# Kernel tuning notes

Measured on AMD Instinct MI355X. Metric: run time of the kernel, lower is better.

Reference implementation:

```python
import jax, jax.numpy as jnp
import numpy as np

INPUT_DIM = 1024; HID = 512; DSTATE = 64; EXPAND = 2; HDIM = 32; NHEAD = 8; DFF = 1024
DIN = EXPAND * HID          # 1024 inner dim
NH = DIN // HDIM            # 32 heads
G = 1; DCONV = 4            # ngroups, depthwise conv kernel
CONV_DIM = DIN + 2 * G * DSTATE          # 1152 (x, B, C go through conv)
DPROJ = 2 * DIN + 2 * G * DSTATE + NH    # 2208 (z, xBC, dt)
B = 2; L = 4096


def rmsnorm(x, w, eps=1e-5):
    return x * jax.lax.rsqrt(jnp.mean(x * x, axis=-1, keepdims=True) + eps) * w


def layernorm(x, w, b, eps=1e-5):
    m = jnp.mean(x, axis=-1, keepdims=True)
    v = jnp.mean((x - m) ** 2, axis=-1, keepdims=True)
    return (x - m) * jax.lax.rsqrt(v + eps) * w + b


def mamba_block(x, Wi, cw, cb, dtb, Alog, Dp, nw, Wo):
    # Mamba-2 style selective scan block (SISO, ngroups=1)
    Bb, Ln, _ = x.shape
    zxbcdt = x @ Wi                                   # [B,L,DPROJ]
    z = zxbcdt[..., :DIN]
    xBC = zxbcdt[..., DIN:DIN + CONV_DIM]
    dt = zxbcdt[..., DIN + CONV_DIM:]                 # [B,L,NH]
    # causal depthwise conv1d + silu
    xBC = jnp.transpose(xBC, (0, 2, 1))               # [B,C,L]
    xBC = jax.lax.conv_general_dilated(xBC, cw, (1,), [(DCONV - 1, 0)],
                                       feature_group_count=CONV_DIM) + cb[None, :, None]
    xBC = jax.nn.silu(jnp.transpose(xBC, (0, 2, 1)))
    xs = xBC[..., :DIN].reshape(Bb, Ln, NH, HDIM)     # [B,L,H,P]
    Bm = xBC[..., DIN:DIN + DSTATE]                   # [B,L,N]
    Cm = xBC[..., DIN + DSTATE:]                      # [B,L,N]
    dt = jax.nn.softplus(dt + dtb)                    # [B,L,H]
    decay = jnp.exp(dt * (-jnp.exp(Alog)))            # [B,L,H]
    dtx = dt[..., None] * xs                          # [B,L,H,P]

    def step(h, inp):
        dec, dx, Bt, Ct = inp                         # [B,H],[B,H,P],[B,N],[B,N]
        h = h * dec[:, :, None, None] + dx[..., None] * Bt[:, None, None, :]
        return h, jnp.einsum('bhpn,bn->bhp', h, Ct)

    h0 = jnp.zeros((Bb, NH, HDIM, DSTATE), x.dtype)
    _, ys = jax.lax.scan(step, h0, (jnp.moveaxis(decay, 1, 0), jnp.moveaxis(dtx, 1, 0),
                                    jnp.moveaxis(Bm, 1, 0), jnp.moveaxis(Cm, 1, 0)))
    y = jnp.moveaxis(ys, 0, 1) + Dp[None, None, :, None] * xs
    y = y.reshape(Bb, Ln, DIN)
    return rmsnorm(y * jax.nn.silu(z), nw) @ Wo       # gated RMSNorm + out proj


def transformer_layer(x, Wqkv, bqkv, Wo, bo, W1, b1, W2, b2, ln1w, ln1b, ln2w, ln2b):
    Bb, Ln, Dm = x.shape
    hd = Dm // NHEAD
    qkv = x @ Wqkv + bqkv
    q, k, v = jnp.split(qkv, 3, axis=-1)
    sp = lambda t: t.reshape(Bb, Ln, NHEAD, hd).transpose(0, 2, 1, 3)
    q, k, v = sp(q), sp(k), sp(v)
    att = jax.nn.softmax(jnp.einsum('bhqd,bhkd->bhqk', q, k) / np.float32(np.sqrt(hd)), axis=-1)
    o = jnp.einsum('bhqk,bhkd->bhqd', att, v).transpose(0, 2, 1, 3).reshape(Bb, Ln, Dm)
    x = layernorm(x + o @ Wo + bo, ln1w, ln1b)
    ff = jax.nn.gelu(x @ W1 + b1, approximate=False) @ W2 + b2
    return layernorm(x + ff, ln2w, ln2b)


def setup_inputs() -> dict:
    key = jax.random.key(0)
    ks = iter(jax.random.split(key, 64))
    w = lambda shape, s=0.02: jax.random.normal(next(ks), shape, jnp.float32) * s
    d = {}
    d['x'] = jax.random.normal(next(ks), (B, L, INPUT_DIM), jnp.float32)
    d['Wp'] = w((INPUT_DIM, HID)); d['bp'] = jnp.zeros((HID,), jnp.float32)
    for p in ('m1', 'm2'):
        d[p + '_Wi'] = w((HID, DPROJ))
        d[p + '_cw'] = w((CONV_DIM, 1, DCONV), 0.2)
        d[p + '_cb'] = jnp.zeros((CONV_DIM,), jnp.float32)
        d[p + '_dtb'] = jnp.log(jnp.expm1(jax.random.uniform(next(ks), (NH,), jnp.float32, 0.001, 0.1)))
        d[p + '_Alog'] = jnp.log(jax.random.uniform(next(ks), (NH,), jnp.float32, 1.0, 16.0))
        d[p + '_D'] = jnp.ones((NH,), jnp.float32)
        d[p + '_nw'] = jnp.ones((DIN,), jnp.float32)
        d[p + '_Wo'] = w((DIN, HID))
    d['n1_w'] = jnp.ones((HID,), jnp.float32); d['n2_w'] = jnp.ones((HID,), jnp.float32)
    d['ds_w'] = w((HID, HID, 3)); d['ds_b'] = jnp.zeros((HID,), jnp.float32)
    d['t_Wqkv'] = w((HID, 3 * HID)); d['t_bqkv'] = jnp.zeros((3 * HID,), jnp.float32)
    d['t_Wo'] = w((HID, HID)); d['t_bo'] = jnp.zeros((HID,), jnp.float32)
    d['t_W1'] = w((HID, DFF)); d['t_b1'] = jnp.zeros((DFF,), jnp.float32)
    d['t_W2'] = w((DFF, HID)); d['t_b2'] = jnp.zeros((HID,), jnp.float32)
    d['t_ln1w'] = jnp.ones((HID,), jnp.float32); d['t_ln1b'] = jnp.zeros((HID,), jnp.float32)
    d['t_ln2w'] = jnp.ones((HID,), jnp.float32); d['t_ln2b'] = jnp.zeros((HID,), jnp.float32)
    d['on_w'] = jnp.ones((HID,), jnp.float32); d['on_b'] = jnp.zeros((HID,), jnp.float32)
    return d


def reference(x, Wp, bp,
              m1_Wi, m1_cw, m1_cb, m1_dtb, m1_Alog, m1_D, m1_nw, m1_Wo,
              m2_Wi, m2_cw, m2_cb, m2_dtb, m2_Alog, m2_D, m2_nw, m2_Wo,
              n1_w, n2_w, ds_w, ds_b,
              t_Wqkv, t_bqkv, t_Wo, t_bo, t_W1, t_b1, t_W2, t_b2,
              t_ln1w, t_ln1b, t_ln2w, t_ln2b, on_w, on_b):
    x = x @ Wp + bp
    x = rmsnorm(mamba_block(x, m1_Wi, m1_cw, m1_cb, m1_dtb, m1_Alog, m1_D, m1_nw, m1_Wo) + x, n1_w)
    x = rmsnorm(mamba_block(x, m2_Wi, m2_cw, m2_cb, m2_dtb, m2_Alog, m2_D, m2_nw, m2_Wo) + x, n2_w)
    xt = jnp.transpose(x, (0, 2, 1))                  # [B,HID,L]
    xt = jax.lax.conv_general_dilated(xt, ds_w, (2,), [(1, 1)]) + ds_b[None, :, None]
    x = jnp.transpose(xt, (0, 2, 1))                  # [B,L/2,HID]
    x = transformer_layer(x, t_Wqkv, t_bqkv, t_Wo, t_bo, t_W1, t_b1, t_W2, t_b2,
                          t_ln1w, t_ln1b, t_ln2w, t_ln2b)
    return layernorm(x, on_w, on_b)
```

## Files before the change

### kernel.cpp

```cpp
#include <hip/hip_runtime.h>
#include <math.h>

#define DIN_   1024
#define DSTATE_ 64
#define NH_    32
#define HDIM_  32
#define CONVD_ 1152
#define DPROJ_ 2208
#define HID_   512
#define LSEQ_  4096
#define BB_    2
#define LT_    2048
#define NHEAD_ 8
#define HD_    64
#define DFF_   1024
#define LC_    256
#define NC_    16
#define NS_    2
#define KTS_   (LT_ / 64 / NS_)

typedef __attribute__((ext_vector_type(8))) short bf16x8;
typedef __attribute__((ext_vector_type(4))) short s16x4;
typedef __attribute__((ext_vector_type(4))) float f32x4;

__device__ __forceinline__ float siluf(float x) { return x / (1.f + __expf(-x)); }

__device__ __forceinline__ short f2b(float f) {
  union { float f; unsigned u; } v; v.f = f;
  unsigned r = (v.u + 0x7fffu + ((v.u >> 16) & 1u)) >> 16;
  return (short)r;
}

__device__ __forceinline__ short f2bt(float f) {
  union { float f; unsigned u; } v; v.f = f;
  return (short)(v.u >> 16);
}

__device__ __forceinline__ float b2f(short s) {
  union { unsigned u; float f; } v; v.u = ((unsigned)(unsigned short)s) << 16;
  return v.f;
}

__device__ __forceinline__ void gload16(const short* g, short* lds_base) {
#if __has_builtin(__builtin_amdgcn_global_load_lds)
  __builtin_amdgcn_global_load_lds((const __attribute__((address_space(1))) void*)g,
                                   (__attribute__((address_space(3))) void*)lds_base, 16, 0, 0);
#else
  int l = threadIdx.x & 63;
  ((bf16x8*)lds_base)[l] = *(const bf16x8*)g;
#endif
}

__device__ __forceinline__ void xcd_swz(int& bx, int& by, int& bz) {
  int nbx = gridDim.x, nby = gridDim.y;
  int nwg = nbx * nby * gridDim.z;
  int orig = (blockIdx.z * nby + blockIdx.y) * nbx + blockIdx.x;
  int q = nwg >> 3, r = nwg & 7;
  int xcd = orig & 7, lin = orig >> 3;
  int wg = (xcd < r ? xcd * (q + 1) : r * (q + 1) + (xcd - r) * q) + lin;
  bx = wg % nbx; wg /= nbx;
  by = wg % nby;
  bz = wg / nby;
}

__global__ void ec_f2b(const float* __restrict__ in, short* __restrict__ out, int n8)
{
  int i = blockIdx.x * 256 + threadIdx.x;
  if (i >= n8) return;
  const float4* p = (const float4*)(in + (size_t)i * 8);
  float4 a = p[0], b = p[1];
  bf16x8 o;
  o[0] = f2b(a.x); o[1] = f2b(a.y); o[2] = f2b(a.z); o[3] = f2b(a.w);
  o[4] = f2b(b.x); o[5] = f2b(b.y); o[6] = f2b(b.z); o[7] = f2b(b.w);
  *(bf16x8*)(out + (size_t)i * 8) = o;
}

__global__ __launch_bounds__(256) void ec_w2bt(const float* __restrict__ W,
                                               short* __restrict__ Wt, int K, int N)
{
  __shared__ float t[32][33];
  int k0 = blockIdx.x * 32, n0 = blockIdx.y * 32;
  int tx = threadIdx.x & 31, ty = threadIdx.x >> 5;
#pragma unroll
  for (int i = 0; i < 32; i += 8) t[ty + i][tx] = W[(size_t)(k0 + ty + i) * N + n0 + tx];
  __syncthreads();
#pragma unroll
  for (int i = 0; i < 32; i += 8) Wt[(size_t)(n0 + ty + i) * K + k0 + tx] = f2b(t[tx][ty + i]);
}

__global__ void ec_dswt(const float* __restrict__ w, short* __restrict__ wt)
{
  int idx = blockIdx.x * 256 + threadIdx.x;
  if (idx >= HID_ * 1536) return;
  int o = idx / 1536, r = idx % 1536;
  int k = r >> 9, i = r & 511;
  wt[idx] = f2b(w[((size_t)o * HID_ + i) * 3 + k]);
}

__global__ void ec_cwt(const float* __restrict__ cw, float* __restrict__ cwt)
{
  int idx = blockIdx.x * 256 + threadIdx.x;
  if (idx >= CONVD_ * 4) return;
  int j = idx / CONVD_, c = idx % CONVD_;
  cwt[idx] = cw[c * 4 + j];
}

__global__ __launch_bounds__(256) void ec_gemm16b(
    const short* __restrict__ A, const short* __restrict__ Wt,
    const float* __restrict__ bias, const float* __restrict__ res,
    float* __restrict__ Cf, short* __restrict__ Ch,
    int M, int N, int K, int act, int lda, long Az, int Mz)
{
  __shared__ short As_[2][2048];
  __shared__ short Bs_[2][2048];
  int bxi, byi, bzi;
  xcd_swz(bxi, byi, bzi);
  A += (size_t)bzi * Az;
  const int mz = bzi * Mz;
  const int tid = threadIdx.x;
  const int l = tid & 63, w = tid >> 6;
  const int m0 = byi * 64, n0 = bxi * 64;
  const int wm = (w >> 1) * 32, wn = (w & 1) * 32;
  const int lr = l & 15, lk = l >> 4;
  const int arow = l >> 2, acol = (l & 3) * 8;

  f32x4 acc[2][2];
#pragma unroll
  for (int i = 0; i < 2; ++i)
#pragma unroll
    for (int j = 0; j < 2; ++j) acc[i][j] = f32x4{0.f, 0.f, 0.f, 0.f};

  {
    const short* ga = A + (size_t)(m0 + w * 16 + arow) * lda + acol;
    int rb = n0 + w * 16 + arow; if (rb > N - 1) rb = N - 1;
    const short* gb = Wt + (size_t)rb * K + acol;
    gload16(ga, &As_[0][w * 512]);
    gload16(gb, &Bs_[0][w * 512]);
  }

  const int KT = K >> 5;
  for (int kt = 0; kt < KT; ++kt) {
    __syncthreads();
    if (kt + 1 < KT) {
      int k0 = (kt + 1) << 5;
      int nb = (kt + 1) & 1;
      const short* ga = A + (size_t)(m0 + w * 16 + arow) * lda + k0 + acol;
      int rb = n0 + w * 16 + arow; if (rb > N - 1) rb = N - 1;
      const short* gb = Wt + (size_t)rb * K + k0 + acol;
      gload16(ga, &As_[nb][w * 512]);
      gload16(gb, &Bs_[nb][w * 512]);
    }
    int cb = kt & 1;
    bf16x8 af[2], bfv[2];
#pragma unroll
    for (int mf = 0; mf < 2; ++mf)
      af[mf] = *(const bf16x8*)&As_[cb][(wm + mf * 16 + lr) * 32 + lk * 8];
#pragma unroll
    for (int nf = 0; nf < 2; ++nf)
      bfv[nf] = *(const bf16x8*)&Bs_[cb][(wn + nf * 16 + lr) * 32 + lk * 8];
#pragma unroll
    for (int mf = 0; mf < 2; ++mf)
#pragma unroll
      for (int nf = 0; nf < 2; ++nf)
        acc[mf][nf] = __builtin_amdgcn_mfma_f32_16x16x32_bf16(af[mf], bfv[nf], acc[mf][nf], 0, 0, 0);
  }

#pragma unroll
  for (int mf = 0; mf < 2; ++mf)
#pragma unroll
    for (int nf = 0; nf < 2; ++nf)
#pragma unroll
      for (int r = 0; r < 4; ++r) {
        int m = mz + m0 + wm + mf * 16 + lk * 4 + r;
        int n = n0 + wn + nf * 16 + lr;
        if (n < N) {
          float v = acc[mf][nf][r];
          if (bias) v += bias[n];
          if (act == 1) v = 0.5f * v * (1.f + erff(v * 0.70710678118f));
          if (res) v += res[(size_t)m * N + n];
          if (Cf) Cf[(size_t)m * N + n] = v;
          if (Ch) Ch[(size_t)m * N + n] = f2b(v);
        }
      }
}

static inline void gemm16b(hipStream_t s, const short* A, const short* Wt, const float* bias,
                           const float* res, float* Cf, short* Ch, int M, int N, int K, int act) {
  dim3 g((N + 63) / 64, M / 64), b(256);
  ec_gemm16b<<<g, b, 0, s>>>(A, Wt, bias, res, Cf, Ch, M, N, K, act, K, 0, 0);
}

__global__ __launch_bounds__(512) void ec_dsfix(
    const short* __restrict__ x16, const short* __restrict__ wt,
    const float* __restrict__ bias, float* __restrict__ dsf, short* __restrict__ ds16)
{
  const int b = blockIdx.x, o = threadIdx.x;
  float v = bias[o];
#pragma unroll
  for (int k = 1; k < 3; ++k) {
    const short* xr = x16 + ((size_t)b * LSEQ_ + (k - 1)) * HID_;
    const short* wr = wt + (size_t)o * 1536 + k * 512;
    for (int i = 0; i < 512; ++i) v += b2f(xr[i]) * b2f(wr[i]);
  }
  dsf[(size_t)b * LT_ * HID_ + o] = v;
  ds16[(size_t)b * LT_ * HID_ + o] = f2b(v);
}

__global__ __launch_bounds__(256) void ec_conv1d_silu(
    const short* __restrict__ zx16, const float* __restrict__ cwt,
    const float* __restrict__ cb, short* __restrict__ xbc16,
    short* __restrict__ B16, short* __restrict__ C16)
{
  int idx = blockIdx.x * 256 + threadIdx.x;
  const int NG = CONVD_ / 4;
  if (idx >= BB_ * LSEQ_ * NG) return;
  int cg = idx % NG;
  int row = idx / NG;
  int l = row & (LSEQ_ - 1);
  int c0 = cg * 4;
  float4 cbv = *(const float4*)(cb + c0);
  float a0 = cbv.x, a1 = cbv.y, a2 = cbv.z, a3 = cbv.w;
#pragma unroll
  for (int j = 0; j < 4; ++j) {
    int ll = l - 3 + j;
    if (ll >= 0) {
      s16x4 xv = *(const s16x4*)(zx16 + (size_t)(row + ll - l) * DPROJ_ + DIN_ + c0);
      float4 wv = *(const float4*)(cwt + j * CONVD_ + c0);
      a0 += b2f(xv[0]) * wv.x;
      a1 += b2f(xv[1]) * wv.y;
      a2 += b2f(xv[2]) * wv.z;
      a3 += b2f(xv[3]) * wv.w;
    }
  }
  a0 = siluf(a0); a1 = siluf(a1); a2 = siluf(a2); a3 = siluf(a3);
  s16x4 pk; pk[0] = f2b(a0); pk[1] = f2b(a1); pk[2] = f2b(a2); pk[3] = f2b(a3);
  *(s16x4*)(xbc16 + (size_t)row * CONVD_ + c0) = pk;
  if (c0 >= DIN_) {
    int col = c0 - DIN_;
    if (col < 64) *(s16x4*)(B16 + (size_t)row * 64 + col) = pk;
    else          *(s16x4*)(C16 + (size_t)row * 64 + col - 64) = pk;
  }
}

__global__ __launch_bounds__(256) void ec_ssd_cumsum(
    const short* __restrict__ zx16, const float* __restrict__ dtb,
    const float* __restrict__ Alog, float* __restrict__ dts,
    float* __restrict__ lp, float* __restrict__ Pc)
{
  const int c = blockIdx.x, b = blockIdx.y, hg = blockIdx.z;
  const int t = threadIdx.x;
  const int lane = t & 63, wv = t >> 6;
  const size_t row = (size_t)b * LSEQ_ + (size_t)c * LC_ + t;
  const int h0 = hg * 8;
  __shared__ float wsum[4][8];

  bf16x8 dv = *(const bf16x8*)(zx16 + row * DPROJ_ + (DIN_ + CONVD_) + h0);
  float dt[8], cs[8];
#pragma unroll
  for (int j = 0; j < 8; ++j) {
    float x = b2f(dv[j]) + dtb[h0 + j];
    float sp = (x > 20.f) ? x : log1pf(__expf(x));
    dt[j] = sp;
    cs[j] = sp;
  }
#pragma unroll
  for (int d = 1; d < 64; d <<= 1) {
#pragma unroll
    for (int j = 0; j < 8; ++j) {
      float o = __shfl_up(cs[j], d, 64);
      if (lane >= d) cs[j] += o;
    }
  }
  if (lane == 63)
#pragma unroll
    for (int j = 0; j < 8; ++j) wsum[wv][j] = cs[j];
  __syncthreads();
#pragma unroll
  for (int j = 0; j < 8; ++j) {
    float base = 0.f;
#pragma unroll
    for (int k = 0; k < 3; ++k) if (k < wv) base += wsum[k][j];
    cs[j] += base;
  }
#pragma unroll
  for (int j = 0; j < 8; ++j) {
    int h = h0 + j;
    float lpv = -expf(Alog[h]) * cs[j];
    dts[row * NH_ + h] = dt[j];
    lp[row * NH_ + h] = lpv;
    if (t == LC_ - 1) Pc[(b * NC_ + c) * NH_ + h] = expf(lpv);
  }
}

__global__ __launch_bounds__(64) void ec_vt(
    const short* __restrict__ xbc16, const float* __restrict__ dts, short* __restrict__ VT)
{
  const int h = blockIdx.x, c = blockIdx.y, b = blockIdx.z;
  const int l = threadIdx.x;
  const size_t rowB = (size_t)b * LSEQ_ + (size_t)c * LC_;
  const size_t vtbase = (size_t)((b * NC_ + c) * NH_ + h) * 32;
  __shared__ float tile[32][33];
  for (int tt = 0; tt < 8; ++tt) {
#pragma unroll
    for (int i = 0; i < 16; ++i) {
      int r = i * 2 + (l >> 5);
      size_t row = rowB + tt * 32 + r;
      tile[r][l & 31] = b2f(xbc16[row * CONVD_ + h * 32 + (l & 31)]) * dts[row * NH_ + h];
    }
    __syncthreads();
#pragma unroll
    for (int j = 0; j < 16; ++j) {
      int p = j * 2 + (l >> 5);
      VT[(vtbase + p) * 256 + tt * 32 + (l & 31)] = f2b(tile[l & 31][p]);
    }
    __syncthreads();
  }
}

__device__ __forceinline__ float* state_ptr(float* stbuf, int b, int c, int h, int e)
{
  return stbuf + ((size_t)((b * NC_ + c) * NH_ + h)) * 2048 + e;
}

__global__ __launch_bounds__(64) void ec_ssd_p1(
    const short* __restrict__ B16, const short* __restrict__ VT,
    const float* __restrict__ lp, float* __restrict__ stbuf)
{
  const int h = blockIdx.x, c = blockIdx.y, b = blockIdx.z;
  const int l = threadIdx.x, lr = l & 15, lk = l >> 4;
  const size_t rowB = (size_t)b * LSEQ_ + (size_t)c * LC_;
  const size_t vtbase = (size_t)((b * NC_ + c) * NH_ + h) * 32;
  __shared__ short BT[64][264];
  for (int i = 0; i < 4; ++i) {
    int t = i * 64 + l;
#pragma unroll
    for (int g = 0; g < 8; ++g) {
      bf16x8 v = *(const bf16x8*)&B16[(rowB + t) * 64 + g * 8];
#pragma unroll
      for (int j = 0; j < 8; ++j) BT[g * 8 + j][t] = v[j];
    }
  }
  __syncthreads();
  const float lpE = lp[(rowB + LC_ - 1) * NH_ + h];
  f32x4 acc[2][4];
#pragma unroll
  for (int i = 0; i < 2; ++i)
#pragma unroll
    for (int j = 0; j < 4; ++j) acc[i][j] = f32x4{0.f, 0.f, 0.f, 0.f};

  for (int ks = 0; ks < 8; ++ks) {
    float wv[8];
#pragma unroll
    for (int j = 0; j < 8; ++j) {
      int t = ks * 32 + lk * 8 + j;
      wv[j] = __expf(lpE - lp[(rowB + t) * NH_ + h]);
    }
    bf16x8 af[2];
#pragma unroll
    for (int mf = 0; mf < 2; ++mf) {
      bf16x8 v = *(const bf16x8*)&VT[(vtbase + mf * 16 + lr) * 256 + ks * 32 + lk * 8];
#pragma unroll
      for (int j = 0; j < 8; ++j) af[mf][j] = f2b(b2f(v[j]) * wv[j]);
    }
#pragma unroll
    for (int nf = 0; nf < 4; ++nf) {
      bf16x8 bf = *(const bf16x8*)&BT[nf * 16 + lr][ks * 32 + lk * 8];
#pragma unroll
      for (int mf = 0; mf < 2; ++mf)
        acc[mf][nf] = __builtin_amdgcn_mfma_f32_16x16x32_bf16(af[mf], bf, acc[mf][nf], 0, 0, 0);
    }
  }
#pragma unroll
  for (int mf = 0; mf < 2; ++mf)
#pragma unroll
    for (int nf = 0; nf < 4; ++nf)
#pragma unroll
      for (int r = 0; r < 4; ++r) {
        int p = mf * 16 + lk * 4 + r, n = nf * 16 + lr;
        *state_ptr(stbuf, b, c, h, p * 64 + n) = acc[mf][nf][r];
      }
}

__global__ __launch_bounds__(512) void ec_scan_p2(
    float* __restrict__ stbuf, const float* __restrict__ Pc)
{
  const int h = blockIdx.x, b = blockIdx.y;
  const int tid = threadIdx.x;
  const int e = (tid >> 4) * 64 + (tid & 15) * 4;
  float h0 = 0.f, h1 = 0.f, h2 = 0.f, h3 = 0.f;
  for (int c = 0; c < NC_; ++c) {
    float* ptr = state_ptr(stbuf, b, c, h, e);
    float4 S = *(float4*)ptr;
    *(float4*)ptr = make_float4(h0, h1, h2, h3);
    float P = Pc[(b * NC_ + c) * NH_ + h];
    h0 = h0 * P + S.x;
    h1 = h1 * P + S.y;
    h2 = h2 * P + S.z;
    h3 = h3 * P + S.w;
  }
}

__global__ __launch_bounds__(256) void ec_ssd_p3(
    const short* __restrict__ B16, const short* __restrict__ C16,
    const short* __restrict__ VT, const float* __restrict__ lp,
    const short* __restrict__ xbc16, const float* __restrict__ Dp,
    float* __restrict__ stbuf, short* __restrict__ y16)
{
  const int h = blockIdx.x, c = blockIdx.y, b = blockIdx.z;
  const int tid = threadIdx.x;
  const int w = tid >> 6, l = tid & 63, lr = l & 15, lk = l >> 4;
  const size_t rowB = (size_t)b * LSEQ_ + (size_t)c * LC_;
  const size_t vtbase = (size_t)((b * NC_ + c) * NH_ + h) * 32;
  __shared__ short hI[32][72];
  __shared__ short Pl[4][64][72];

  for (int i = tid; i < 2048; i += 256)
    hI[i >> 6][i & 63] = f2b(*state_ptr(stbuf, b, c, h, i));
  __syncthreads();

  const int t0 = w * 64;
  bf16x8 cf[4][2];
#pragma unroll
  for (int tf = 0; tf < 4; ++tf)
#pragma unroll
    for (int ks = 0; ks < 2; ++ks)
      cf[tf][ks] = *(const bf16x8*)&C16[(rowB + t0 + tf * 16 + lr) * 64 + ks * 32 + lk * 8];

  f32x4 Y[4][2];
#pragma unroll
  for (int i = 0; i < 4; ++i)
#pragma unroll
    for (int j = 0; j < 2; ++j) Y[i][j] = f32x4{0.f, 0.f, 0.f, 0.f};
#pragma unroll
  for (int nf = 0; nf < 2; ++nf)
#pragma unroll
    for (int ks = 0; ks < 2; ++ks) {
      bf16x8 hf = *(const bf16x8*)&hI[nf * 16 + lr][ks * 32 + lk * 8];
#pragma unroll
      for (int mf = 0; mf < 4; ++mf)
        Y[mf][nf] = __builtin_amdgcn_mfma_f32_16x16x32_bf16(cf[mf][ks], hf, Y[mf][nf], 0, 0, 0);
    }
#pragma unroll
  for (int mf = 0; mf < 4; ++mf)
#pragma unroll
    for (int r = 0; r < 4; ++r) {
      float e = __expf(lp[(rowB + t0 + mf * 16 + lk * 4 + r) * NH_ + h]);
      Y[mf][0][r] *= e;
      Y[mf][1][r] *= e;
    }
  float tlp[4];
#pragma unroll
  for (int tf = 0; tf < 4; ++tf)
    tlp[tf] = lp[(rowB + t0 + tf * 16 + lr) * NH_ + h];

  for (int st = 0; st <= w; ++st) {
    const int s0 = st * 64;
#pragma unroll
    for (int half = 0; half < 2; ++half) {
      f32x4 ST[2][4];
#pragma unroll
      for (int i = 0; i < 2; ++i)
#pragma unroll
        for (int j = 0; j < 4; ++j) ST[i][j] = f32x4{0.f, 0.f, 0.f, 0.f};
#pragma unroll
      for (int sf2 = 0; sf2 < 2; ++sf2) {
        int sf = half * 2 + sf2;
#pragma unroll
        for (int ks = 0; ks < 2; ++ks) {
          bf16x8 bfr = *(const bf16x8*)&B16[(rowB + s0 + sf * 16 + lr) * 64 + ks * 32 + lk * 8];
#pragma unroll
          for (int tf = 0; tf < 4; ++tf)
            ST[sf2][tf] = __builtin_amdgcn_mfma_f32_16x16x32_bf16(bfr, cf[tf][ks], ST[sf2][tf], 0, 0, 0);
        }
      }
#pragma unroll
      for (int sf2 = 0; sf2 < 2; ++sf2) {
        int sf = half * 2 + sf2;
        float slp[4];
#pragma unroll
        for (int r = 0; r < 4; ++r)
          slp[r] = lp[(rowB + s0 + sf * 16 + lk * 4 + r) * NH_ + h];
#pragma unroll
        for (int tf = 0; tf < 4; ++tf) {
          float pv[4];
#pragma unroll
          for (int r = 0; r < 4; ++r) {
            pv[r] = ST[sf2][tf][r] * __expf(tlp[tf] - slp[r]);
            if (st == w && (sf * 16 + lk * 4 + r) > (tf * 16 + lr)) pv[r] = 0.f;
          }
          union { float f; unsigned u; } q0, q1, q2, q3;
          q0.f = pv[0]; q1.f = pv[1]; q2.f = pv[2]; q3.f = pv[3];
          uint2 pk;
          pk.x = (q0.u >> 16) | (q1.u & 0xffff0000u);
          pk.y = (q2.u >> 16) | (q3.u & 0xffff0000u);
          *(uint2*)&Pl[w][tf * 16 + lr][sf * 16 + lk * 4] = pk;
        }
      }
    }
    __builtin_amdgcn_sched_barrier(0);
    asm volatile("s_waitcnt lgkmcnt(0)" ::: "memory");
    __builtin_amdgcn_sched_barrier(0);
#pragma unroll
    for (int ks = 0; ks < 2; ++ks) {
      bf16x8 vf[2];
#pragma unroll
      for (int nf = 0; nf < 2; ++nf)
        vf[nf] = *(const bf16x8*)&VT[(vtbase + nf * 16 + lr) * 256 + s0 + ks * 32 + lk * 8];
#pragma unroll
      for (int mf = 0; mf < 4; ++mf) {
        bf16x8 pf = *(const bf16x8*)&Pl[w][mf * 16 + lr][ks * 32 + lk * 8];
#pragma unroll
        for (int nf = 0; nf < 2; ++nf)
          Y[mf][nf] = __builtin_amdgcn_mfma_f32_16x16x32_bf16(pf, vf[nf], Y[mf][nf], 0, 0, 0);
      }
    }
  }
  const float Dh = Dp[h];
#pragma unroll
  for (int mf = 0; mf < 4; ++mf)
#pragma unroll
    for (int r = 0; r < 4; ++r) {
      size_t yrow = rowB + t0 + mf * 16 + lk * 4 + r;
#pragma unroll
      for (int nf = 0; nf < 2; ++nf) {
        float xv = b2f(xbc16[yrow * CONVD_ + h * 32 + nf * 16 + lr]);
        y16[yrow * DIN_ + h * 32 + nf * 16 + lr] = f2b(Y[mf][nf][r] + Dh * xv);
      }
    }
}

__global__ __launch_bounds__(256) void ec_gate_rms16(
    const short* __restrict__ y16, const short* __restrict__ zx16,
    const float* __restrict__ nw, short* __restrict__ out)
{
  const int row = blockIdx.x;
  const int c0 = threadIdx.x * 4;
  s16x4 yv = *(const s16x4*)(y16 + (size_t)row * DIN_ + c0);
  s16x4 zv = *(const s16x4*)(zx16 + (size_t)row * DPROJ_ + c0);
  float v[4]; float ss = 0.f;
#pragma unroll
  for (int j = 0; j < 4; ++j) {
    float t = b2f(yv[j]) * siluf(b2f(zv[j]));
    v[j] = t; ss += t * t;
  }
#pragma unroll
  for (int m = 32; m >= 1; m >>= 1) ss += __shfl_xor(ss, m, 64);
  __shared__ float buf[4];
  if ((threadIdx.x & 63) == 0) buf[threadIdx.x >> 6] = ss;
  __syncthreads();
  ss = buf[0] + buf[1] + buf[2] + buf[3];
  float scale = rsqrtf(ss / (float)DIN_ + 1e-5f);
  float4 wv = *(const float4*)(nw + c0);
  s16x4 ov;
  ov[0] = f2b(v[0] * scale * wv.x);
  ov[1] = f2b(v[1] * scale * wv.y);
  ov[2] = f2b(v[2] * scale * wv.z);
  ov[3] = f2b(v[3] * scale * wv.w);
  *(s16x4*)(out + (size_t)row * DIN_ + c0) = ov;
}

__global__ __launch_bounds__(128) void ec_rmsadd16(
    const float* __restrict__ a, const float* __restrict__ bres,
    const float* __restrict__ w, float* __restrict__ out, short* __restrict__ out16)
{
  const int row = blockIdx.x;
  const float* ar = a + (size_t)row * HID_;
  const float* br = bres + (size_t)row * HID_;
  float v[4]; float ss = 0.f;
#pragma unroll
  for (int j = 0; j < 4; ++j) {
    int c = j * 128 + threadIdx.x;
    float t = ar[c] + br[c];
    v[j] = t; ss += t * t;
  }
#pragma unroll
  for (int m = 32; m >= 1; m >>= 1) ss += __shfl_xor(ss, m, 64);
  __shared__ float buf[2];
  if ((threadIdx.x & 63) == 0) buf[threadIdx.x >> 6] = ss;
  __syncthreads();
  ss = buf[0] + buf[1];
  float scale = rsqrtf(ss / (float)HID_ + 1e-5f);
#pragma unroll
  for (int j = 0; j < 4; ++j) {
    int c = j * 128 + threadIdx.x;
    float o = v[j] * scale * w[c];
    out[(size_t)row * HID_ + c] = o;
    out16[(size_t)row * HID_ + c] = f2b(o);
  }
}

__global__ __launch_bounds__(128) void ec_ln16(
    const float* __restrict__ in, const float* __restrict__ w,
    const float* __restrict__ bb, float* __restrict__ out, short* __restrict__ out16)
{
  const int row = blockIdx.x;
  const float* ir = in + (size_t)row * HID_;
  float v[4]; float s = 0.f, s2 = 0.f;
#pragma unroll
  for (int j = 0; j < 4; ++j) {
    int c = j * 128 + threadIdx.x;
    float t = ir[c];
    v[j] = t; s += t; s2 += t * t;
  }
#pragma unroll
  for (int m = 32; m >= 1; m >>= 1) { s += __shfl_xor(s, m, 64); s2 += __shfl_xor(s2, m, 64); }
  __shared__ float buf[4];
  if ((threadIdx.x & 63) == 0) { int wi = threadIdx.x >> 6; buf[wi * 2] = s; buf[wi * 2 + 1] = s2; }
  __syncthreads();
  s = buf[0] + buf[2]; s2 = buf[1] + buf[3];
  float mean = s / (float)HID_;
  float var = s2 / (float)HID_ - mean * mean;
  float inv = rsqrtf(var + 1e-5f);
#pragma unroll
  for (int j = 0; j < 4; ++j) {
    int c = j * 128 + threadIdx.x;
    float o = (v[j] - mean) * inv * w[c] + bb[c];
    out[(size_t)row * HID_ + c] = o;
    if (out16) out16[(size_t)row * HID_ + c] = f2b(o);
  }
}

__global__ __launch_bounds__(256) void ec_attn16(
    const short* __restrict__ qkv, float* __restrict__ Op, float2* __restrict__ ml)
{
  const int b = blockIdx.z & 1, split = blockIdx.z >> 1;
  const int h = blockIdx.y, qt = blockIdx.x;
  __shared__ short Kl[64 * 68];
  __shared__ short Vl[64 * 68];
  __shared__ short Pl[64 * 68];
  const int tid = threadIdx.x;
  const int l = tid & 63, w = tid >> 6;
  const int lr = l & 15, lk = l >> 4;

  const size_t qrow = (size_t)b * LT_ + qt * 64 + w * 16 + lr;
  bf16x8 qf[2];
  qf[0] = *(const bf16x8*)&qkv[qrow * 1536 + h * HD_ + lk * 8];
  qf[1] = *(const bf16x8*)&qkv[qrow * 1536 + h * HD_ + lk * 8 + 32];

  float mrun[4] = {-INFINITY, -INFINITY, -INFINITY, -INFINITY};
  float lsum[4] = {0.f, 0.f, 0.f, 0.f};
  f32x4 O[4];
#pragma unroll
  for (int df = 0; df < 4; ++df) O[df] = f32x4{0.f, 0.f, 0.f, 0.f};

  const int krow = tid >> 2, kcg = (tid & 3) * 16;
  const int vd = tid & 63, vw = tid >> 6;

  for (int kt = split * KTS_; kt < (split + 1) * KTS_; ++kt) {
    const size_t krbase = (size_t)b * LT_ + kt * 64;
    {
      const short* kp = &qkv[(krbase + krow) * 1536 + HID_ + h * HD_ + kcg];
      *(bf16x8*)&Kl[krow * 68 + kcg] = *(const bf16x8*)kp;
      *(bf16x8*)&Kl[krow * 68 + kcg + 8] = *(const bf16x8*)(kp + 8);
    }
#pragma unroll
    for (int kk = 0; kk < 4; ++kk) {
      int key0 = vw * 16 + kk * 4;
      s16x4 pk;
#pragma unroll
      for (int j = 0; j < 4; ++j)
        pk[j] = qkv[(krbase + key0 + j) * 1536 + 2 * HID_ + h * HD_ + vd];
      *(s16x4*)&Vl[vd * 68 + key0] = pk;
    }
    __syncthreads();

    f32x4 S[4];
#pragma unroll
    for (int nf = 0; nf < 4; ++nf) S[nf] = f32x4{0.f, 0.f, 0.f, 0.f};
#pragma unroll
    for (int ks = 0; ks < 2; ++ks)
#pragma unroll
      for (int nf = 0; nf < 4; ++nf) {
        bf16x8 kb = *(const bf16x8*)&Kl[(nf * 16 + lr) * 68 + ks * 32 + lk * 8];
        S[nf] = __builtin_amdgcn_mfma_f32_16x16x32_bf16(qf[ks], kb, S[nf], 0, 0, 0);
      }

    float fr[4];
#pragma unroll
    for (int r = 0; r < 4; ++r) {
      float mt = fmaxf(fmaxf(S[0][r], S[1][r]), fmaxf(S[2][r], S[3][r])) * 0.125f;
      mt = fmaxf(mt, __shfl_xor(mt, 1));
      mt = fmaxf(mt, __shfl_xor(mt, 2));
      mt = fmaxf(mt, __shfl_xor(mt, 4));
      mt = fmaxf(mt, __shfl_xor(mt, 8));
      float mn = fmaxf(mrun[r], mt);
      fr[r] = __expf(mrun[r] - mn);
      mrun[r] = mn;
      lsum[r] *= fr[r];
    }
#pragma unroll
    for (int nf = 0; nf < 4; ++nf)
#pragma unroll
      for (int r = 0; r < 4; ++r) {
        float p = __expf(S[nf][r] * 0.125f - mrun[r]);
        lsum[r] += p;
        Pl[(w * 16 + lk * 4 + r) * 68 + nf * 16 + lr] = f2bt(p);
      }
#pragma unroll
    for (int df = 0; df < 4; ++df) {
      O[df][0] *= fr[0]; O[df][1] *= fr[1]; O[df][2] *= fr[2]; O[df][3] *= fr[3];
    }

#pragma unroll
    for (int ks = 0; ks < 2; ++ks) {
      bf16x8 pa = *(const bf16x8*)&Pl[(w * 16 + lr) * 68 + ks * 32 + lk * 8];
#pragma unroll
      for (int df = 0; df < 4; ++df) {
        bf16x8 vb = *(const bf16x8*)&Vl[(df * 16 + lr) * 68 + ks * 32 + lk * 8];
        O[df] = __builtin_amdgcn_mfma_f32_16x16x32_bf16(pa, vb, O[df], 0, 0, 0);
      }
    }
    __syncthreads();
  }

#pragma unroll
  for (int r = 0; r < 4; ++r) {
    lsum[r] += __shfl_xor(lsum[r], 1);
    lsum[r] += __shfl_xor(lsum[r], 2);
    lsum[r] += __shfl_xor(lsum[r], 4);
    lsum[r] += __shfl_xor(lsum[r], 8);
  }
  const size_t sstride = (size_t)BB_ * NHEAD_ * LT_;
  const size_t obase = (size_t)split * sstride + ((size_t)b * NHEAD_ + h) * LT_ + qt * 64 + w * 16;
#pragma unroll
  for (int df = 0; df < 4; ++df)
#pragma unroll
    for (int r = 0; r < 4; ++r)
      Op[(obase + lk * 4 + r) * 64 + df * 16 + lr] = O[df][r];
  if (lr == 0)
#pragma unroll
    for (int r = 0; r < 4; ++r)
      ml[obase + lk * 4 + r] = make_float2(mrun[r], lsum[r]);
}

__global__ __launch_bounds__(256) void ec_attn_comb(
    const float* __restrict__ Op, const float2* __restrict__ ml, short* __restrict__ out)
{
  const int qt = blockIdx.x, h = blockIdx.y, b = blockIdx.z;
  const int r = threadIdx.x >> 2, c0 = (threadIdx.x & 3) * 16;
  const int qrow = qt * 64 + r;
  const size_t sstride = (size_t)BB_ * NHEAD_ * LT_;
  const size_t rb = ((size_t)b * NHEAD_ + h) * LT_ + qrow;
  float m[NS_], lv[NS_];
  float mmax = -INFINITY;
#pragma unroll
  for (int s = 0; s < NS_; ++s) {
    float2 v = ml[rb + s * sstride];
    m[s] = v.x; lv[s] = v.y;
    mmax = fmaxf(mmax, m[s]);
  }
  float den = 0.f, wsc[NS_];
#pragma unroll
  for (int s = 0; s < NS_; ++s) { wsc[s] = __expf(m[s] - mmax); den += lv[s] * wsc[s]; }
  float inv = 1.f / den;
  float o[16];
#pragma unroll
  for (int i = 0; i < 16; ++i) o[i] = 0.f;
#pragma unroll
  for (int s = 0; s < NS_; ++s) {
    const float* p = Op + (rb + s * sstride) * 64 + c0;
    float wq = wsc[s];
#pragma unroll
    for (int i = 0; i < 4; ++i) {
      float4 v = *(const float4*)(p + i * 4);
      o[i * 4 + 0] += v.x * wq; o[i * 4 + 1] += v.y * wq;
      o[i * 4 + 2] += v.z * wq; o[i * 4 + 3] += v.w * wq;
    }
  }
  short* op = out + ((size_t)b * LT_ + qrow) * HID_ + h * HD_ + c0;
#pragma unroll
  for (int i = 0; i < 16; ++i) op[i] = f2b(o[i] * inv);
}

extern "C" void kernel_launch(void* const* d_in, const int* in_sizes, int n_in,
                              void* d_out, int out_size, void* d_ws, size_t ws_size,
                              hipStream_t stream)
{
  const float* x_in   = (const float*)d_in[0];
  const float* Wp     = (const float*)d_in[1];
  const float* bp     = (const float*)d_in[2];
  const float* m_Wi[2]   = {(const float*)d_in[3],  (const float*)d_in[11]};
  const float* m_cw[2]   = {(const float*)d_in[4],  (const float*)d_in[12]};
  const float* m_cb[2]   = {(const float*)d_in[5],  (const float*)d_in[13]};
  const float* m_dtb[2]  = {(const float*)d_in[6],  (const float*)d_in[14]};
  const float* m_Alog[2] = {(const float*)d_in[7],  (const float*)d_in[15]};
  const float* m_D[2]    = {(const float*)d_in[8],  (const float*)d_in[16]};
  const float* m_nw[2]   = {(const float*)d_in[9],  (const float*)d_in[17]};
  const float* m_Wo[2]   = {(const float*)d_in[10], (const float*)d_in[18]};
  const float* n_w[2]    = {(const float*)d_in[19], (const float*)d_in[20]};
  const float* ds_w   = (const float*)d_in[21];
  const float* ds_b   = (const float*)d_in[22];
  const float* t_Wqkv = (const float*)d_in[23];
  const float* t_bqkv = (const float*)d_in[24];
  const float* t_Wo   = (const float*)d_in[25];
  const float* t_bo   = (const float*)d_in[26];
  const float* t_W1   = (const float*)d_in[27];
  const float* t_b1   = (const float*)d_in[28];
  const float* t_W2   = (const float*)d_in[29];
  const float* t_b2   = (const float*)d_in[30];
  const float* t_ln1w = (const float*)d_in[31];
  const float* t_ln1b = (const float*)d_in[32];
  const float* t_ln2w = (const float*)d_in[33];
  const float* t_ln2b = (const float*)d_in[34];
  const float* on_w   = (const float*)d_in[35];
  const float* on_b   = (const float*)d_in[36];

  char* ws = (char*)d_ws;
  float* bx    = (float*)(ws + 0);
  short* zx16  = (short*)(ws + 16777216);
  float* stbuf = (float*)(ws + 16777216 + 36175872);
  short* xbc16 = (short*)(ws + 89128960);
  short* y16   = (short*)(ws + 126877696);
  short* VT    = (short*)(ws + 143654912);
  float* lp    = (float*)(ws + 160432128);
  float* dts   = (float*)(ws + 161480704);
  short* wslot = (short*)(ws + 162529280);
  float* Pc    = (float*)(ws + 165150720);
  float* cwt   = (float*)(ws + 165154816);

  short* B16 = wslot;
  short* C16 = wslot + 524288;
  float* byf = (float*)(ws + 126877696);

  short* x16     = (short*)(ws + 126877696);
  short* bx16    = (short*)(ws + 89128960);
  short* gated16 = (short*)(ws + 89128960 + 18874368);

  float*  Opart = (float*)(ws + 89128960);
  float2* mlbuf = (float2*)(ws + 89128960 + 33554432);

  char* tzone = ws + 16777216;
  short* ds16  = (short*)tzone;
  float* dsf   = (float*)(tzone + 4194304);
  short* qkv16 = (short*)(tzone + 12582912);
  short* att16 = (short*)(tzone + 25165824);
  float* bt1   = (float*)(tzone + 29360128);
  short* ln116 = (short*)(tzone + 37748736);
  float* bxt2  = (float*)(tzone + 41943040);
  short* ff16  = (short*)(tzone + 50331648);
  float* bt2   = (float*)(tzone + 58720256);
  float* bxt3  = (float*)(ws + 89128960);

  const int MR = BB_ * LSEQ_;
  const int MT = BB_ * LT_;

  ec_f2b<<<(MR * 1024 / 8 + 255) / 256, 256, 0, stream>>>(x_in, x16, MR * 1024 / 8);
  ec_w2bt<<<dim3(1024 / 32, 512 / 32), 256, 0, stream>>>(Wp, wslot, 1024, 512);
  gemm16b(stream, x16, wslot, bp, nullptr, bx, bx16, MR, HID_, 1024, 0);

  for (int blk = 0; blk < 2; ++blk) {
    ec_w2bt<<<dim3(512 / 32, 2208 / 32), 256, 0, stream>>>(m_Wi[blk], wslot, 512, 2208);
    gemm16b(stream, bx16, wslot, nullptr, nullptr, nullptr, zx16, MR, DPROJ_, HID_, 0);
    ec_cwt<<<(CONVD_ * 4 + 255) / 256, 256, 0, stream>>>(m_cw[blk], cwt);
    ec_conv1d_silu<<<(MR * (CONVD_ / 4) + 255) / 256, 256, 0, stream>>>(
        zx16, cwt, m_cb[blk], xbc16, B16, C16);
    ec_ssd_cumsum<<<dim3(NC_, BB_, NH_ / 8), 256, 0, stream>>>(zx16, m_dtb[blk], m_Alog[blk], dts, lp, Pc);
    ec_vt<<<dim3(NH_, NC_, BB_), 64, 0, stream>>>(xbc16, dts, VT);
    ec_ssd_p1<<<dim3(NH_, NC_, BB_), 64, 0, stream>>>(B16, VT, lp, stbuf);
    ec_scan_p2<<<dim3(NH_, BB_), 512, 0, stream>>>(stbuf, Pc);
    ec_ssd_p3<<<dim3(NH_, NC_, BB_), 256, 0, stream>>>(B16, C16, VT, lp, xbc16, m_D[blk], stbuf, y16);
    ec_gate_rms16<<<MR, 256, 0, stream>>>(y16, zx16, m_nw[blk], gated16);
    ec_w2bt<<<dim3(1024 / 32, 512 / 32), 256, 0, stream>>>(m_Wo[blk], wslot, 1024, 512);
    gemm16b(stream, gated16, wslot, nullptr, nullptr, byf, nullptr, MR, HID_, DIN_, 0);
    ec_rmsadd16<<<MR, 128, 0, stream>>>(byf, bx, n_w[blk], bx, bx16);
  }

  ec_dswt<<<(HID_ * 1536 + 255) / 256, 256, 0, stream>>>(ds_w, wslot);
  {
    dim3 g(512 / 64, LT_ / 64, BB_), b(256);
    ec_gemm16b<<<g, b, 0, stream>>>(bx16 - 512, wslot, ds_b, nullptr, dsf, ds16,
                                    LT_, HID_, 1536, 0, 1024, (long)LSEQ_ * HID_, LT_);
  }
  ec_dsfix<<<BB_, 512, 0, stream>>>(bx16, wslot, ds_b, dsf, ds16);

  ec_w2bt<<<dim3(512 / 32, 1536 / 32), 256, 0, stream>>>(t_Wqkv, wslot, 512, 1536);
  gemm16b(stream, ds16, wslot, t_bqkv, nullptr, nullptr, qkv16, MT, 3 * HID_, HID_, 0);
  ec_attn16<<<dim3(LT_ / 64, NHEAD_, BB_ * NS_), 256, 0, stream>>>(qkv16, Opart, mlbuf);
  ec_attn_comb<<<dim3(LT_ / 64, NHEAD_, BB_), 256, 0, stream>>>(Opart, mlbuf, att16);
  ec_w2bt<<<dim3(512 / 32, 512 / 32), 256, 0, stream>>>(t_Wo, wslot, 512, 512);
  gemm16b(stream, att16, wslot, t_bo, dsf, bt1, nullptr, MT, HID_, HID_, 0);
  ec_ln16<<<MT, 128, 0, stream>>>(bt1, t_ln1w, t_ln1b, bxt2, ln116);
  ec_w2bt<<<dim3(512 / 32, 1024 / 32), 256, 0, stream>>>(t_W1, wslot, 512, 1024);
  gemm16b(stream, ln116, wslot, t_b1, nullptr, nullptr, ff16, MT, DFF_, HID_, 1);
  ec_w2bt<<<dim3(1024 / 32, 512 / 32), 256, 0, stream>>>(t_W2, wslot, 1024, 512);
  gemm16b(stream, ff16, wslot, t_b2, bxt2, bt2, nullptr, MT, HID_, DFF_, 0);
  ec_ln16<<<MT, 128, 0, stream>>>(bt2, t_ln2w, t_ln2b, bxt3, nullptr);
  ec_ln16<<<MT, 128, 0, stream>>>(bxt3, on_w, on_b, (float*)d_out, nullptr);
}
```

Baseline: 640.0 us.

## Skip attention rescale when max unchanged; bf16 out-proj output; vectorize rmsadd

The attention kernel now skips the running-max update and accumulator rescale whenever every score in the wave stays within a margin of the current max. It also replaces -INFINITY initial values with -1e30 so the result stays finite. The Mamba out-projection GEMM writes bf16 instead of fp32, and the residual RMSNorm reads it with vectorized loads and stores. These cut exp/shuffle work and memory traffic, at the cost of extra precision loss from rounding the projection output to bf16 before the residual add.

```diff
diff --git a/kernel.cpp b/kernel.cpp
--- a/kernel.cpp
+++ b/kernel.cpp
@@ -560,19 +560,18 @@
 }
 
 __global__ __launch_bounds__(128) void ec_rmsadd16(
-    const float* __restrict__ a, const float* __restrict__ bres,
+    const short* __restrict__ a16, const float* __restrict__ bres,
     const float* __restrict__ w, float* __restrict__ out, short* __restrict__ out16)
 {
   const int row = blockIdx.x;
-  const float* ar = a + (size_t)row * HID_;
-  const float* br = bres + (size_t)row * HID_;
+  const int c0 = threadIdx.x * 4;
+  s16x4 av = *(const s16x4*)(a16 + (size_t)row * HID_ + c0);
+  float4 brv = *(const float4*)(bres + (size_t)row * HID_ + c0);
   float v[4]; float ss = 0.f;
-#pragma unroll
-  for (int j = 0; j < 4; ++j) {
-    int c = j * 128 + threadIdx.x;
-    float t = ar[c] + br[c];
-    v[j] = t; ss += t * t;
-  }
+  v[0] = b2f(av[0]) + brv.x; v[1] = b2f(av[1]) + brv.y;
+  v[2] = b2f(av[2]) + brv.z; v[3] = b2f(av[3]) + brv.w;
+#pragma unroll
+  for (int j = 0; j < 4; ++j) ss += v[j] * v[j];
 #pragma unroll
   for (int m = 32; m >= 1; m >>= 1) ss += __shfl_xor(ss, m, 64);
   __shared__ float buf[2];
@@ -580,13 +579,12 @@
   __syncthreads();
   ss = buf[0] + buf[1];
   float scale = rsqrtf(ss / (float)HID_ + 1e-5f);
-#pragma unroll
-  for (int j = 0; j < 4; ++j) {
-    int c = j * 128 + threadIdx.x;
-    float o = v[j] * scale * w[c];
-    out[(size_t)row * HID_ + c] = o;
-    out16[(size_t)row * HID_ + c] = f2b(o);
-  }
+  float4 wv = *(const float4*)(w + c0);
+  float o0 = v[0] * scale * wv.x, o1 = v[1] * scale * wv.y;
+  float o2 = v[2] * scale * wv.z, o3 = v[3] * scale * wv.w;
+  *(float4*)(out + (size_t)row * HID_ + c0) = make_float4(o0, o1, o2, o3);
+  s16x4 ov; ov[0] = f2b(o0); ov[1] = f2b(o1); ov[2] = f2b(o2); ov[3] = f2b(o3);
+  *(s16x4*)(out16 + (size_t)row * HID_ + c0) = ov;
 }
 
 __global__ __launch_bounds__(128) void ec_ln16(
@@ -637,7 +635,7 @@
   qf[0] = *(const bf16x8*)&qkv[qrow * 1536 + h * HD_ + lk * 8];
   qf[1] = *(const bf16x8*)&qkv[qrow * 1536 + h * HD_ + lk * 8 + 32];
 
-  float mrun[4] = {-INFINITY, -INFINITY, -INFINITY, -INFINITY};
+  float mrun[4] = {-1e30f, -1e30f, -1e30f, -1e30f};
   float lsum[4] = {0.f, 0.f, 0.f, 0.f};
   f32x4 O[4];
 #pragma unroll
@@ -675,18 +673,30 @@
         S[nf] = __builtin_amdgcn_mfma_f32_16x16x32_bf16(qf[ks], kb, S[nf], 0, 0, 0);
       }
 
-    float fr[4];
-#pragma unroll
-    for (int r = 0; r < 4; ++r) {
-      float mt = fmaxf(fmaxf(S[0][r], S[1][r]), fmaxf(S[2][r], S[3][r])) * 0.125f;
-      mt = fmaxf(mt, __shfl_xor(mt, 1));
-      mt = fmaxf(mt, __shfl_xor(mt, 2));
-      mt = fmaxf(mt, __shfl_xor(mt, 4));
-      mt = fmaxf(mt, __shfl_xor(mt, 8));
-      float mn = fmaxf(mrun[r], mt);
-      fr[r] = __expf(mrun[r] - mn);
-      mrun[r] = mn;
-      lsum[r] *= fr[r];
+    int ok = 1;
+#pragma unroll
+    for (int nf = 0; nf < 4; ++nf)
+#pragma unroll
+      for (int r = 0; r < 4; ++r)
+        ok &= (S[nf][r] * 0.125f <= mrun[r] + 8.f);
+    if (!__all(ok)) {
+      float fr[4];
+#pragma unroll
+      for (int r = 0; r < 4; ++r) {
+        float mt = fmaxf(fmaxf(S[0][r], S[1][r]), fmaxf(S[2][r], S[3][r])) * 0.125f;
+        mt = fmaxf(mt, __shfl_xor(mt, 1));
+        mt = fmaxf(mt, __shfl_xor(mt, 2));
+        mt = fmaxf(mt, __shfl_xor(mt, 4));
+        mt = fmaxf(mt, __shfl_xor(mt, 8));
+        float mn = fmaxf(mrun[r], mt);
+        fr[r] = __expf(mrun[r] - mn);
+        mrun[r] = mn;
+        lsum[r] *= fr[r];
+      }
+#pragma unroll
+      for (int df = 0; df < 4; ++df) {
+        O[df][0] *= fr[0]; O[df][1] *= fr[1]; O[df][2] *= fr[2]; O[df][3] *= fr[3];
+      }
     }
 #pragma unroll
     for (int nf = 0; nf < 4; ++nf)
@@ -696,10 +706,6 @@
         lsum[r] += p;
         Pl[(w * 16 + lk * 4 + r) * 68 + nf * 16 + lr] = f2bt(p);
       }
-#pragma unroll
-    for (int df = 0; df < 4; ++df) {
-      O[df][0] *= fr[0]; O[df][1] *= fr[1]; O[df][2] *= fr[2]; O[df][3] *= fr[3];
-    }
 
 #pragma unroll
     for (int ks = 0; ks < 2; ++ks) {
@@ -742,7 +748,7 @@
   const size_t sstride = (size_t)BB_ * NHEAD_ * LT_;
   const size_t rb = ((size_t)b * NHEAD_ + h) * LT_ + qrow;
   float m[NS_], lv[NS_];
-  float mmax = -INFINITY;
+  float mmax = -1e30f;
 #pragma unroll
   for (int s = 0; s < NS_; ++s) {
     float2 v = ml[rb + s * sstride];
@@ -820,7 +826,7 @@
 
   short* B16 = wslot;
   short* C16 = wslot + 524288;
-  float* byf = (float*)(ws + 126877696);
+  short* a16buf = (short*)(ws + 126877696);
 
   short* x16     = (short*)(ws + 126877696);
   short* bx16    = (short*)(ws + 89128960);
@@ -861,8 +867,8 @@
     ec_ssd_p3<<<dim3(NH_, NC_, BB_), 256, 0, stream>>>(B16, C16, VT, lp, xbc16, m_D[blk], stbuf, y16);
     ec_gate_rms16<<<MR, 256, 0, stream>>>(y16, zx16, m_nw[blk], gated16);
     ec_w2bt<<<dim3(1024 / 32, 512 / 32), 256, 0, stream>>>(m_Wo[blk], wslot, 1024, 512);
-    gemm16b(stream, gated16, wslot, nullptr, nullptr, byf, nullptr, MR, HID_, DIN_, 0);
-    ec_rmsadd16<<<MR, 128, 0, stream>>>(byf, bx, n_w[blk], bx, bx16);
+    gemm16b(stream, gated16, wslot, nullptr, nullptr, nullptr, a16buf, MR, HID_, DIN_, 0);
+    ec_rmsadd16<<<MR, 128, 0, stream>>>(a16buf, bx, n_w[blk], bx, bx16);
   }
 
   ec_dswt<<<(HID_ * 1536 + 255) / 256, 256, 0, stream>>>(ds_w, wslot);
```

New measurement: 623.9 us. 1.03x faster.
